# Kernel tuning notes

Measured on AMD Instinct MI355X. Metric: run time of the kernel, lower is better.

Reference implementation:

```python
import jax, jax.numpy as jnp
import numpy as np

N, E, B = 50000, 640000, 4
H, L = 128, 4
NODE_IN, EDGE_IN, COND_IN, NODE_OUT = 12, 4, 10, 3


def _mlp(x, w1, b1, w2, b2):
    # Linear -> ReLU -> Linear
    return jnp.maximum(x @ w1 + b1, 0.0) @ w2 + b2


def setup_inputs() -> dict:
    key = jax.random.key(0)
    keys = iter(jax.random.split(key, 64))

    def p(*shape):
        fan_in = shape[-2] if len(shape) >= 2 else shape[-1]
        return (jax.random.normal(next(keys), shape, jnp.float32) / np.sqrt(fan_in)).astype(jnp.float32)

    inp = {
        "x": jax.random.normal(next(keys), (N, NODE_IN), jnp.float32),
        "edge_index": jax.random.randint(next(keys), (2, E), 0, N),
        "edge_attr": jax.random.normal(next(keys), (E, EDGE_IN), jnp.float32),
        "conditions": jax.random.normal(next(keys), (B, COND_IN), jnp.float32),
        "batch": jnp.sort(jax.random.randint(next(keys), (N,), 0, B)),
        # encoders
        "enc_node_w1": p(NODE_IN, H), "enc_node_b1": jnp.zeros((H,), jnp.float32),
        "enc_node_w2": p(H, H), "enc_node_b2": jnp.zeros((H,), jnp.float32),
        "enc_edge_w1": p(EDGE_IN, H), "enc_edge_b1": jnp.zeros((H,), jnp.float32),
        "enc_edge_w2": p(H, H), "enc_edge_b2": jnp.zeros((H,), jnp.float32),
        "enc_cond_w1": p(COND_IN, H), "enc_cond_b1": jnp.zeros((H,), jnp.float32),
        "enc_cond_w2": p(H, H), "enc_cond_b2": jnp.zeros((H,), jnp.float32),
        # shared MultiheadAttention: with a single key, softmax weight == 1 per head,
        # so output = out_proj(v_proj(kv)); q/k projections cancel exactly (and have
        # identically zero gradient), so only v/out projections are materialized.
        "attn_wv": p(H, H), "attn_bv": jnp.zeros((H,), jnp.float32),
        "attn_wo": p(H, H), "attn_bo": jnp.zeros((H,), jnp.float32),
        # processor layers (stacked over L)
        "pe_w1": p(L, 4 * H, H), "pe_b1": jnp.zeros((L, H), jnp.float32),
        "pe_w2": p(L, H, H), "pe_b2": jnp.zeros((L, H), jnp.float32),
        "pn_w1": p(L, 3 * H, H), "pn_b1": jnp.zeros((L, H), jnp.float32),
        "pn_w2": p(L, H, H), "pn_b2": jnp.zeros((L, H), jnp.float32),
        # decoder
        "dec_w1": p(H, H), "dec_b1": jnp.zeros((H,), jnp.float32),
        "dec_w2": p(H, NODE_OUT), "dec_b2": jnp.zeros((NODE_OUT,), jnp.float32),
    }
    return inp


def reference(x, edge_index, edge_attr, conditions, batch,
              enc_node_w1, enc_node_b1, enc_node_w2, enc_node_b2,
              enc_edge_w1, enc_edge_b1, enc_edge_w2, enc_edge_b2,
              enc_cond_w1, enc_cond_b1, enc_cond_w2, enc_cond_b2,
              attn_wv, attn_bv, attn_wo, attn_bo,
              pe_w1, pe_b1, pe_w2, pe_b2,
              pn_w1, pn_b1, pn_w2, pn_b2,
              dec_w1, dec_b1, dec_w2, dec_b2):
    n = x.shape[0]
    h = _mlp(x, enc_node_w1, enc_node_b1, enc_node_w2, enc_node_b2)           # [N,H]
    e = _mlp(edge_attr, enc_edge_w1, enc_edge_b1, enc_edge_w2, enc_edge_b2)   # [E,H]
    u = _mlp(conditions, enc_cond_w1, enc_cond_b1, enc_cond_w2, enc_cond_b2)  # [B,H]

    row, col = edge_index[0], edge_index[1]
    u_nodes = u[batch]                                                        # [N,H]
    # single-key cross-attention -> softmax over 1 key == 1 -> out_proj(v_proj(u))
    x_cond = (u_nodes @ attn_wv + attn_bv) @ attn_wo + attn_bo               # [N,H], same every layer
    u_edges = u_nodes[row]                                                    # u[batch[row]]

    for l in range(pe_w1.shape[0]):
        # edge update: cat([src, dest, edge_attr, u[batch_e]]) -> MLP
        e = _mlp(jnp.concatenate([h[row], h[col], e, u_edges], axis=1),
                 pe_w1[l], pe_b1[l], pe_w2[l], pe_b2[l])
        # scatter-add aggregation (index_add on row)
        agg = jax.ops.segment_sum(e, row, num_segments=n)                     # [N,H]
        # node update with residual
        h = h + _mlp(jnp.concatenate([h, agg, x_cond], axis=1),
                     pn_w1[l], pn_b1[l], pn_w2[l], pn_b2[l])

    return _mlp(h, dec_w1, dec_b1, dec_w2, dec_b2)                            # [N,node_out]
```

## Files before the change

### kernel.cpp

```cpp
#include <hip/hip_runtime.h>
#include <cstddef>

#define NN 50000
#define NNP 50048
#define NE 640000
#define NB 4
#define H  128
#define NL 4
#define TE 64
#define TEE 128

typedef unsigned int u32;
typedef unsigned short u16;
typedef __attribute__((ext_vector_type(8))) short bf16x8;
typedef __attribute__((ext_vector_type(4))) float f32x4;

__device__ __forceinline__ float bf2f(u16 s) {
    union { u32 u; float f; } v; v.u = ((u32)s) << 16; return v.f;
}
__device__ __forceinline__ u16 f2bf(float f) {
    union { float f; u32 u; } v; v.f = f;
    u32 u = v.u;
    u += 0x7FFF + ((u >> 16) & 1);
    return (u16)(u >> 16);
}
__device__ __forceinline__ void unpack8(uint4 raw, float* d) {
    d[0] = bf2f(raw.x & 0xFFFF); d[1] = bf2f(raw.x >> 16);
    d[2] = bf2f(raw.y & 0xFFFF); d[3] = bf2f(raw.y >> 16);
    d[4] = bf2f(raw.z & 0xFFFF); d[5] = bf2f(raw.z >> 16);
    d[6] = bf2f(raw.w & 0xFFFF); d[7] = bf2f(raw.w >> 16);
}
__device__ __forceinline__ uint4 pack8(const float* s) {
    uint4 pk;
    pk.x = (u32)f2bf(s[0]) | ((u32)f2bf(s[1]) << 16);
    pk.y = (u32)f2bf(s[2]) | ((u32)f2bf(s[3]) << 16);
    pk.z = (u32)f2bf(s[4]) | ((u32)f2bf(s[5]) << 16);
    pk.w = (u32)f2bf(s[6]) | ((u32)f2bf(s[7]) << 16);
    return pk;
}
__device__ __forceinline__ bf16x8 ld_f32_bf8(const float* __restrict__ p) {
    const float4 a = *(const float4*)p;
    const float4 b = *(const float4*)(p + 4);
    bf16x8 r;
    r[0] = (short)f2bf(a.x); r[1] = (short)f2bf(a.y);
    r[2] = (short)f2bf(a.z); r[3] = (short)f2bf(a.w);
    r[4] = (short)f2bf(b.x); r[5] = (short)f2bf(b.y);
    r[6] = (short)f2bf(b.z); r[7] = (short)f2bf(b.w);
    return r;
}

__global__ __launch_bounds__(256) void k_zero(float* __restrict__ p, int n4) {
    const int i = blockIdx.x * 256 + threadIdx.x;
    if (i < n4) ((float4*)p)[i] = make_float4(0.f, 0.f, 0.f, 0.f);
}

__global__ __launch_bounds__(256) void k_hist(const int* __restrict__ rowi,
                                              u32* __restrict__ cnt) {
    const int i = blockIdx.x * 256 + threadIdx.x;
    if (i < NE) atomicAdd(&cnt[rowi[i]], 1u);
}

__global__ __launch_bounds__(1024) void k_scan(u32* __restrict__ cnt) {
    __shared__ u32 part[1024];
    const int t = threadIdx.x;
    const int CHUNK = (NN + 1023) / 1024;
    const int lo = t * CHUNK;
    const int hi = (lo + CHUNK < NN) ? lo + CHUNK : NN;
    u32 s = 0;
    for (int i = lo; i < hi; ++i) s += cnt[i];
    part[t] = s;
    __syncthreads();
    for (int ofs = 1; ofs < 1024; ofs <<= 1) {
        const u32 v = (t >= ofs) ? part[t - ofs] : 0u;
        __syncthreads();
        part[t] += v;
        __syncthreads();
    }
    u32 run = (t == 0) ? 0u : part[t - 1];
    for (int i = lo; i < hi; ++i) { const u32 c = cnt[i]; cnt[i] = run; run += c; }
}

__global__ __launch_bounds__(256) void k_scatter(const int* __restrict__ rowi,
                                                 const int* __restrict__ coli,
                                                 u32* __restrict__ off,
                                                 int* __restrict__ permS,
                                                 int* __restrict__ rowS,
                                                 int* __restrict__ colS) {
    const int i = blockIdx.x * 256 + threadIdx.x;
    if (i < NE) {
        const int r = rowi[i];
        const u32 p = atomicAdd(&off[r], 1u);
        permS[p] = i; rowS[p] = r; colS[p] = coli[i];
    }
}

__global__ __launch_bounds__(256) void k_prep(
    const float* __restrict__ pe_w1, const float* __restrict__ pe_w2,
    const float* __restrict__ pn_w1, const float* __restrict__ pn_w2,
    const float* __restrict__ ew2,   const float* __restrict__ nw2,
    const float* __restrict__ dw1,
    u16* __restrict__ W1t, u16* __restrict__ W2t,
    u16* __restrict__ WaT, u16* __restrict__ WbT,
    u16* __restrict__ Wn1aT, u16* __restrict__ Wn1bT, u16* __restrict__ Wn2T,
    u16* __restrict__ W2et, u16* __restrict__ W2nt, u16* __restrict__ W1dt) {
    const int li = blockIdx.x;
    const float* src; u16* dst;
    switch (blockIdx.y) {
        case 0: src = pe_w1 + ((size_t)li * 512 + 256) * H; dst = W1t  + (size_t)li * H * H; break;
        case 1: src = pe_w2 + (size_t)li * H * H;           dst = W2t  + (size_t)li * H * H; break;
        case 2: src = pe_w1 + (size_t)li * 512 * H;         dst = WaT  + (size_t)li * H * H; break;
        case 3: src = pe_w1 + ((size_t)li * 512 + 128) * H; dst = WbT  + (size_t)li * H * H; break;
        case 4: src = pn_w1 + (size_t)li * 384 * H;         dst = Wn1aT + (size_t)li * H * H; break;
        case 5: src = pn_w1 + ((size_t)li * 384 + 128) * H; dst = Wn1bT + (size_t)li * H * H; break;
        case 6: src = pn_w2 + (size_t)li * H * H;           dst = Wn2T + (size_t)li * H * H; break;
        default:
            if (li == 0)      { src = ew2; dst = W2et; }
            else if (li == 1) { src = nw2; dst = W2nt; }
            else if (li == 2) { src = dw1; dst = W1dt; }
            else return;
            break;
    }
    for (int idx = threadIdx.x; idx < H * H; idx += 256) {
        const int n = idx >> 7, k = idx & 127;
        dst[idx] = f2bf(src[(size_t)k * H + n]);
    }
}

__global__ __launch_bounds__(128) void k_small(
    const float* __restrict__ cond,
    const float* __restrict__ ecw1, const float* __restrict__ ecb1,
    const float* __restrict__ ecw2, const float* __restrict__ ecb2,
    const float* __restrict__ wv, const float* __restrict__ bv,
    const float* __restrict__ wo, const float* __restrict__ bo,
    const float* __restrict__ pe_w1, const float* __restrict__ pe_b1,
    const float* __restrict__ pn_w1, const float* __restrict__ pn_b1,
    float* __restrict__ cbat, float* __restrict__ nbat) {
    __shared__ float tmp[NB][H];
    __shared__ float uL[NB][H];
    __shared__ float xcL[NB][H];
    const int t = threadIdx.x;
    for (int b = 0; b < NB; ++b) {
        float a = ecb1[t];
        for (int k = 0; k < 10; ++k) a = fmaf(cond[b * 10 + k], ecw1[k * H + t], a);
        tmp[b][t] = fmaxf(a, 0.f);
    }
    __syncthreads();
    for (int b = 0; b < NB; ++b) {
        float a = ecb2[t];
        for (int k = 0; k < H; ++k) a = fmaf(tmp[b][k], ecw2[k * H + t], a);
        uL[b][t] = a;
    }
    __syncthreads();
    for (int b = 0; b < NB; ++b) {
        float a = bv[t];
        for (int k = 0; k < H; ++k) a = fmaf(uL[b][k], wv[k * H + t], a);
        tmp[b][t] = a;
    }
    __syncthreads();
    for (int b = 0; b < NB; ++b) {
        float a = bo[t];
        for (int k = 0; k < H; ++k) a = fmaf(tmp[b][k], wo[k * H + t], a);
        xcL[b][t] = a;
    }
    __syncthreads();
    for (int l = 0; l < NL; ++l) {
        const float* w1u = pe_w1 + ((size_t)l * 512 + 384) * H;
        for (int b = 0; b < NB; ++b) {
            float a = pe_b1[l * H + t];
            for (int k = 0; k < H; ++k) a = fmaf(uL[b][k], w1u[k * H + t], a);
            cbat[(l * NB + b) * H + t] = a;
        }
        const float* w1x = pn_w1 + ((size_t)l * 384 + 256) * H;
        for (int b = 0; b < NB; ++b) {
            float a = pn_b1[l * H + t];
            for (int k = 0; k < H; ++k) a = fmaf(xcL[b][k], w1x[k * H + t], a);
            nbat[(l * NB + b) * H + t] = a;
        }
    }
}

__global__ __launch_bounds__(256) void k_enc_e_mfma(
    const float* __restrict__ ea,
    const int* __restrict__ permS,
    const float* __restrict__ w1, const float* __restrict__ b1,
    const u16* __restrict__ W2et, const float* __restrict__ b2,
    u16* __restrict__ e) {
    __shared__ float SI[TE][H + 4];
    const int t = threadIdx.x;
    const long long e0 = (long long)blockIdx.x * TE;
    const int w = t >> 6, l = t & 63;
    const int m16 = l & 15, g = l >> 4;
    const int row = w * 16 + m16;

    const int src = permS[e0 + row];
    const float4 av = *(const float4*)&ea[(size_t)src * 4];

    bf16x8 afrag[4];
#pragma unroll
    for (int ks = 0; ks < 4; ++ks) {
        const int c0 = ks * 32 + g * 8;
        float hv[8];
        {
            const float4 ba = *(const float4*)&b1[c0];
            const float4 bb = *(const float4*)&b1[c0 + 4];
            hv[0] = ba.x; hv[1] = ba.y; hv[2] = ba.z; hv[3] = ba.w;
            hv[4] = bb.x; hv[5] = bb.y; hv[6] = bb.z; hv[7] = bb.w;
        }
#pragma unroll
        for (int k = 0; k < 4; ++k) {
            const float s = (k == 0) ? av.x : (k == 1) ? av.y : (k == 2) ? av.z : av.w;
            const float4 wa = *(const float4*)&w1[k * H + c0];
            const float4 wb = *(const float4*)&w1[k * H + c0 + 4];
            hv[0] = fmaf(s, wa.x, hv[0]); hv[1] = fmaf(s, wa.y, hv[1]);
            hv[2] = fmaf(s, wa.z, hv[2]); hv[3] = fmaf(s, wa.w, hv[3]);
            hv[4] = fmaf(s, wb.x, hv[4]); hv[5] = fmaf(s, wb.y, hv[5]);
            hv[6] = fmaf(s, wb.z, hv[6]); hv[7] = fmaf(s, wb.w, hv[7]);
        }
#pragma unroll
        for (int j = 0; j < 8; ++j) afrag[ks][j] = (short)f2bf(fmaxf(hv[j], 0.f));
    }

    f32x4 acc[8];
#pragma unroll
    for (int nt = 0; nt < 8; ++nt) {
        const float bb = b2[nt * 16 + m16];
        acc[nt][0] = bb; acc[nt][1] = bb; acc[nt][2] = bb; acc[nt][3] = bb;
    }
#pragma unroll
    for (int ks = 0; ks < 4; ++ks) {
#pragma unroll
        for (int nt = 0; nt < 8; ++nt) {
            const bf16x8 bfr =
                *(const bf16x8*)&W2et[(size_t)(nt * 16 + m16) * H + ks * 32 + g * 8];
            acc[nt] = __builtin_amdgcn_mfma_f32_16x16x32_bf16(afrag[ks], bfr, acc[nt], 0, 0, 0);
        }
    }

#pragma unroll
    for (int nt = 0; nt < 8; ++nt)
#pragma unroll
        for (int j = 0; j < 4; ++j)
            SI[w * 16 + g * 4 + j][nt * 16 + m16] = acc[nt][j];
#pragma unroll
    for (int it = 0; it < 4; ++it) {
        const int u = l + it * 64;
        const int j = u >> 4, c8 = (u & 15) * 8;
        *(uint4*)&e[(size_t)(e0 + w * 16 + j) * H + c8] = pack8(&SI[w * 16 + j][c8]);
    }
}

__global__ __launch_bounds__(256) void k_enc_n_mfma(
    const float* __restrict__ x,
    const float* __restrict__ w1, const float* __restrict__ b1,
    const u16* __restrict__ W2nt, const float* __restrict__ b2,
    float* __restrict__ h) {
    __shared__ float SI[TE][H + 4];
    const int t = threadIdx.x;
    const long long n0 = (long long)blockIdx.x * TE;
    const int w = t >> 6, l = t & 63;
    const int m16 = l & 15, g = l >> 4;
    const int row = w * 16 + m16;
    const long long nr = (n0 + row < NN) ? (n0 + row) : (NN - 1);

    float av[12];
    {
        const float4 a0 = *(const float4*)&x[nr * 12];
        const float4 a1 = *(const float4*)&x[nr * 12 + 4];
        const float4 a2 = *(const float4*)&x[nr * 12 + 8];
        av[0] = a0.x; av[1] = a0.y; av[2] = a0.z; av[3] = a0.w;
        av[4] = a1.x; av[5] = a1.y; av[6] = a1.z; av[7] = a1.w;
        av[8] = a2.x; av[9] = a2.y; av[10] = a2.z; av[11] = a2.w;
    }

    bf16x8 afrag[4];
#pragma unroll
    for (int ks = 0; ks < 4; ++ks) {
        const int c0 = ks * 32 + g * 8;
        float hv[8];
        {
            const float4 ba = *(const float4*)&b1[c0];
            const float4 bb = *(const float4*)&b1[c0 + 4];
            hv[0] = ba.x; hv[1] = ba.y; hv[2] = ba.z; hv[3] = ba.w;
            hv[4] = bb.x; hv[5] = bb.y; hv[6] = bb.z; hv[7] = bb.w;
        }
#pragma unroll
        for (int k = 0; k < 12; ++k) {
            const float s = av[k];
            const float4 wa = *(const float4*)&w1[k * H + c0];
            const float4 wb = *(const float4*)&w1[k * H + c0 + 4];
            hv[0] = fmaf(s, wa.x, hv[0]); hv[1] = fmaf(s, wa.y, hv[1]);
            hv[2] = fmaf(s, wa.z, hv[2]); hv[3] = fmaf(s, wa.w, hv[3]);
            hv[4] = fmaf(s, wb.x, hv[4]); hv[5] = fmaf(s, wb.y, hv[5]);
            hv[6] = fmaf(s, wb.z, hv[6]); hv[7] = fmaf(s, wb.w, hv[7]);
        }
#pragma unroll
        for (int j = 0; j < 8; ++j) afrag[ks][j] = (short)f2bf(fmaxf(hv[j], 0.f));
    }

    f32x4 acc[8];
#pragma unroll
    for (int nt = 0; nt < 8; ++nt) {
        const float bb = b2[nt * 16 + m16];
        acc[nt][0] = bb; acc[nt][1] = bb; acc[nt][2] = bb; acc[nt][3] = bb;
    }
#pragma unroll
    for (int ks = 0; ks < 4; ++ks) {
#pragma unroll
        for (int nt = 0; nt < 8; ++nt) {
            const bf16x8 bfr =
                *(const bf16x8*)&W2nt[(size_t)(nt * 16 + m16) * H + ks * 32 + g * 8];
            acc[nt] = __builtin_amdgcn_mfma_f32_16x16x32_bf16(afrag[ks], bfr, acc[nt], 0, 0, 0);
        }
    }

#pragma unroll
    for (int nt = 0; nt < 8; ++nt)
#pragma unroll
        for (int j = 0; j < 4; ++j)
            SI[w * 16 + g * 4 + j][nt * 16 + m16] = acc[nt][j];
    __syncthreads();
    for (int u = t; u < TE * H / 4; u += 256) {
        const int j = u >> 5, c4 = (u & 31) * 4;
        *(float4*)&h[(size_t)(n0 + j) * H + c4] = *(const float4*)&SI[j][c4];
    }
}

__global__ __launch_bounds__(256) void k_gemm_dual_mfma(
    const float* __restrict__ h,
    const u16* __restrict__ WaT, const u16* __restrict__ WbT,
    const float* __restrict__ cbatl, const int* __restrict__ batch,
    u16* __restrict__ Ca, u16* __restrict__ Cb, float* __restrict__ agg) {
    __shared__ u16 SI[TE][H + 8];
    __shared__ float CB[NB][H];
    __shared__ int bL[TE];
    const int t = threadIdx.x;
    const long long n0 = (long long)blockIdx.x * TE;
    const int w = t >> 6, l = t & 63;
    const int m16 = l & 15, g = l >> 4;
    const int row = w * 16 + m16;

    {
        const float4 z4 = make_float4(0.f, 0.f, 0.f, 0.f);
        for (int u = t; u < TE * H / 4; u += 256) {
            const int j = u >> 5, c4 = (u & 31) * 4;
            *(float4*)&agg[(size_t)(n0 + j) * H + c4] = z4;
        }
    }

    if (t < TE) {
        const long long n = n0 + t;
        bL[t] = batch[n < NN ? n : (NN - 1)];
    }
    for (int i = t; i < NB * H; i += 256) ((float*)CB)[i] = cbatl[i];

    bf16x8 afrag[4];
    {
        const float* hp = h + (size_t)(n0 + row) * H + g * 8;
#pragma unroll
        for (int ks = 0; ks < 4; ++ks) afrag[ks] = ld_f32_bf8(hp + ks * 32);
    }
    __syncthreads();

    f32x4 accA[8], accB[8];
#pragma unroll
    for (int nt = 0; nt < 8; ++nt) {
#pragma unroll
        for (int j = 0; j < 4; ++j)
            accA[nt][j] = CB[bL[w * 16 + g * 4 + j]][nt * 16 + m16];
        accB[nt][0] = 0.f; accB[nt][1] = 0.f; accB[nt][2] = 0.f; accB[nt][3] = 0.f;
    }
#pragma unroll
    for (int ks = 0; ks < 4; ++ks) {
#pragma unroll
        for (int nt = 0; nt < 8; ++nt) {
            const size_t off = (size_t)(nt * 16 + m16) * H + ks * 32 + g * 8;
            const bf16x8 ba = *(const bf16x8*)&WaT[off];
            const bf16x8 bb = *(const bf16x8*)&WbT[off];
            accA[nt] = __builtin_amdgcn_mfma_f32_16x16x32_bf16(afrag[ks], ba, accA[nt], 0, 0, 0);
            accB[nt] = __builtin_amdgcn_mfma_f32_16x16x32_bf16(afrag[ks], bb, accB[nt], 0, 0, 0);
        }
    }

#pragma unroll
    for (int s = 0; s < 2; ++s) {
        __syncthreads();
#pragma unroll
        for (int nt = 0; nt < 8; ++nt)
#pragma unroll
            for (int j = 0; j < 4; ++j)
                SI[w * 16 + g * 4 + j][nt * 16 + m16] =
                    f2bf(s ? accB[nt][j] : accA[nt][j]);
        __syncthreads();
        u16* C = s ? Cb : Ca;
        for (int u = t; u < TE * 16; u += 256) {
            const int j = u >> 4, c8 = (u & 15) * 8;
            *(uint4*)&C[(size_t)(n0 + j) * H + c8] = *(const uint4*)&SI[j][c8];
        }
    }
}

template <bool WRITE_E>
__global__ __launch_bounds__(256, 2) void k_edge_mfma(
    const u16* __restrict__ hA, const u16* __restrict__ hB,
    const u16* __restrict__ W1t, const u16* __restrict__ W2t,
    const float* __restrict__ b2,
    const int* __restrict__ rowS, const int* __restrict__ colS,
    u16* __restrict__ e, float* __restrict__ agg) {
    __shared__ u16 SI[TEE][H + 8];
    const int t = threadIdx.x;
    const long long e0 = (long long)blockIdx.x * TEE;
    const int w = t >> 6, l = t & 63;
    const int m16 = l & 15, g = l >> 4;

    bf16x8 af0[4], af1[4];
    {
        const u16* ep0 = e + (size_t)(e0 + w * 32 + m16) * H + g * 8;
        const u16* ep1 = ep0 + 16 * H;
#pragma unroll
        for (int ks = 0; ks < 4; ++ks) {
            af0[ks] = *(const bf16x8*)(ep0 + ks * 32);
            af1[ks] = *(const bf16x8*)(ep1 + ks * 32);
        }
    }

    {
        int rj[8], cj[8];
#pragma unroll
        for (int it = 0; it < 8; ++it) {
            const int j = (l + it * 64) >> 4;
            rj[it] = rowS[e0 + w * 32 + j];
            cj[it] = colS[e0 + w * 32 + j];
        }
        uint4 ga[8], gb[8];
#pragma unroll
        for (int it = 0; it < 8; ++it) {
            const int c8 = ((l + it * 64) & 15) * 8;
            ga[it] = *(const uint4*)&hA[(size_t)rj[it] * H + c8];
            gb[it] = *(const uint4*)&hB[(size_t)cj[it] * H + c8];
        }
#pragma unroll
        for (int it = 0; it < 8; ++it) {
            const int u = l + it * 64;
            const int j = u >> 4, c8 = (u & 15) * 8;
            float va[8], vb[8], sm[8];
            unpack8(ga[it], va);
            unpack8(gb[it], vb);
#pragma unroll
            for (int q = 0; q < 8; ++q) sm[q] = va[q] + vb[q];
            *(uint4*)&SI[w * 32 + j][c8] = pack8(sm);
        }
    }

    f32x4 acc0[8], acc1[8];
#pragma unroll
    for (int nt = 0; nt < 8; ++nt) {
#pragma unroll
        for (int j = 0; j < 4; ++j) {
            acc0[nt][j] = bf2f(SI[w * 32 + g * 4 + j][nt * 16 + m16]);
            acc1[nt][j] = bf2f(SI[w * 32 + 16 + g * 4 + j][nt * 16 + m16]);
        }
    }
#pragma unroll
    for (int ks = 0; ks < 4; ++ks) {
#pragma unroll
        for (int nt = 0; nt < 8; ++nt) {
            const bf16x8 bfr =
                *(const bf16x8*)&W1t[(size_t)(nt * 16 + m16) * H + ks * 32 + g * 8];
            acc0[nt] = __builtin_amdgcn_mfma_f32_16x16x32_bf16(af0[ks], bfr, acc0[nt], 0, 0, 0);
            acc1[nt] = __builtin_amdgcn_mfma_f32_16x16x32_bf16(af1[ks], bfr, acc1[nt], 0, 0, 0);
        }
    }

#pragma unroll
    for (int nt = 0; nt < 8; ++nt)
#pragma unroll
        for (int j = 0; j < 4; ++j) {
            SI[w * 32 + g * 4 + j][nt * 16 + m16]      = f2bf(fmaxf(acc0[nt][j], 0.f));
            SI[w * 32 + 16 + g * 4 + j][nt * 16 + m16] = f2bf(fmaxf(acc1[nt][j], 0.f));
        }

#pragma unroll
    for (int nt = 0; nt < 8; ++nt) {
        const float bb = b2[nt * 16 + m16];
        acc0[nt][0] = bb; acc0[nt][1] = bb; acc0[nt][2] = bb; acc0[nt][3] = bb;
        acc1[nt][0] = bb; acc1[nt][1] = bb; acc1[nt][2] = bb; acc1[nt][3] = bb;
    }
#pragma unroll
    for (int ks = 0; ks < 4; ++ks) {
        const bf16x8 a20 = *(const bf16x8*)&SI[w * 32 + m16][ks * 32 + g * 8];
        const bf16x8 a21 = *(const bf16x8*)&SI[w * 32 + 16 + m16][ks * 32 + g * 8];
#pragma unroll
        for (int nt = 0; nt < 8; ++nt) {
            const bf16x8 bfr =
                *(const bf16x8*)&W2t[(size_t)(nt * 16 + m16) * H + ks * 32 + g * 8];
            acc0[nt] = __builtin_amdgcn_mfma_f32_16x16x32_bf16(a20, bfr, acc0[nt], 0, 0, 0);
            acc1[nt] = __builtin_amdgcn_mfma_f32_16x16x32_bf16(a21, bfr, acc1[nt], 0, 0, 0);
        }
    }

    {
        int r[8];
#pragma unroll
        for (int j = 0; j < 4; ++j) {
            r[j]     = rowS[e0 + w * 32 + g * 4 + j];
            r[4 + j] = rowS[e0 + w * 32 + 16 + g * 4 + j];
        }
#pragma unroll
        for (int nt = 0; nt < 8; ++nt) {
            const int c = nt * 16 + m16;
            float v[8];
#pragma unroll
            for (int j = 0; j < 4; ++j) { v[j] = acc0[nt][j]; v[4 + j] = acc1[nt][j]; }
            float s = v[0];
            int prev = r[0];
#pragma unroll
            for (int j = 1; j < 8; ++j) {
                if (r[j] == prev) s += v[j];
                else { atomicAdd(&agg[(size_t)prev * H + c], s); s = v[j]; prev = r[j]; }
            }
            atomicAdd(&agg[(size_t)prev * H + c], s);
        }
    }

    if (WRITE_E) {
#pragma unroll
        for (int nt = 0; nt < 8; ++nt)
#pragma unroll
            for (int j = 0; j < 4; ++j) {
                SI[w * 32 + g * 4 + j][nt * 16 + m16]      = f2bf(acc0[nt][j]);
                SI[w * 32 + 16 + g * 4 + j][nt * 16 + m16] = f2bf(acc1[nt][j]);
            }
#pragma unroll
        for (int it = 0; it < 8; ++it) {
            const int u = l + it * 64;
            const int j = u >> 4, c8 = (u & 15) * 8;
            *(uint4*)&e[(size_t)(e0 + w * 32 + j) * H + c8] = *(const uint4*)&SI[w * 32 + j][c8];
        }
    }
}

__global__ __launch_bounds__(256) void k_node_mfma(
    const u16* __restrict__ Wn1aT, const u16* __restrict__ Wn1bT,
    const u16* __restrict__ Wn2T, const float* __restrict__ bn2,
    const float* __restrict__ nbatl, const int* __restrict__ batch,
    const float* __restrict__ agg, float* __restrict__ h) {
    __shared__ float SI[TE][H + 4];
    const int t = threadIdx.x;
    const long long n0 = (long long)blockIdx.x * TE;
    const int w = t >> 6, l = t & 63;
    const int m16 = l & 15, g = l >> 4;
    const int row = w * 16 + m16;

    bf16x8 afrag[4];
    {
        const float* hp = h + (size_t)(n0 + row) * H + g * 8;
#pragma unroll
        for (int ks = 0; ks < 4; ++ks) afrag[ks] = ld_f32_bf8(hp + ks * 32);
    }

    int bj[4];
#pragma unroll
    for (int j = 0; j < 4; ++j) {
        const long long n = n0 + w * 16 + g * 4 + j;
        bj[j] = batch[n < NN ? n : (NN - 1)];
    }

    f32x4 acc[8];
#pragma unroll
    for (int nt = 0; nt < 8; ++nt)
#pragma unroll
        for (int j = 0; j < 4; ++j)
            acc[nt][j] = nbatl[(size_t)bj[j] * H + nt * 16 + m16];

#pragma unroll
    for (int ks = 0; ks < 4; ++ks)
#pragma unroll
        for (int nt = 0; nt < 8; ++nt) {
            const bf16x8 bfr =
                *(const bf16x8*)&Wn1aT[(size_t)(nt * 16 + m16) * H + ks * 32 + g * 8];
            acc[nt] = __builtin_amdgcn_mfma_f32_16x16x32_bf16(afrag[ks], bfr, acc[nt], 0, 0, 0);
        }

    {
        const float* ap = agg + (size_t)(n0 + row) * H + g * 8;
#pragma unroll
        for (int ks = 0; ks < 4; ++ks) afrag[ks] = ld_f32_bf8(ap + ks * 32);
    }
#pragma unroll
    for (int ks = 0; ks < 4; ++ks)
#pragma unroll
        for (int nt = 0; nt < 8; ++nt) {
            const bf16x8 bfr =
                *(const bf16x8*)&Wn1bT[(size_t)(nt * 16 + m16) * H + ks * 32 + g * 8];
            acc[nt] = __builtin_amdgcn_mfma_f32_16x16x32_bf16(afrag[ks], bfr, acc[nt], 0, 0, 0);
        }

#pragma unroll
    for (int nt = 0; nt < 8; ++nt)
#pragma unroll
        for (int j = 0; j < 4; ++j)
            SI[w * 16 + g * 4 + j][nt * 16 + m16] = fmaxf(acc[nt][j], 0.f);

#pragma unroll
    for (int nt = 0; nt < 8; ++nt) {
        const float bb = bn2[nt * 16 + m16];
        acc[nt][0] = bb; acc[nt][1] = bb; acc[nt][2] = bb; acc[nt][3] = bb;
    }
#pragma unroll
    for (int ks = 0; ks < 4; ++ks) {
        bf16x8 a2;
        const float* hp = &SI[w * 16 + m16][ks * 32 + g * 8];
#pragma unroll
        for (int j = 0; j < 8; ++j) a2[j] = (short)f2bf(hp[j]);
#pragma unroll
        for (int nt = 0; nt < 8; ++nt) {
            const bf16x8 bfr =
                *(const bf16x8*)&Wn2T[(size_t)(nt * 16 + m16) * H + ks * 32 + g * 8];
            acc[nt] = __builtin_amdgcn_mfma_f32_16x16x32_bf16(a2, bfr, acc[nt], 0, 0, 0);
        }
    }

#pragma unroll
    for (int nt = 0; nt < 8; ++nt)
#pragma unroll
        for (int j = 0; j < 4; ++j)
            SI[w * 16 + g * 4 + j][nt * 16 + m16] = acc[nt][j];

#pragma unroll
    for (int it = 0; it < 8; ++it) {
        const int u = l + it * 64;
        const int j = u >> 5, c4 = (u & 31) * 4;
        float4 hv = *(const float4*)&h[(size_t)(n0 + w * 16 + j) * H + c4];
        const float4 sv = *(const float4*)&SI[w * 16 + j][c4];
        hv.x += sv.x; hv.y += sv.y; hv.z += sv.z; hv.w += sv.w;
        *(float4*)&h[(size_t)(n0 + w * 16 + j) * H + c4] = hv;
    }
}

__global__ __launch_bounds__(256) void k_dec_mfma(
    const float* __restrict__ h,
    const u16* __restrict__ W1dt, const float* __restrict__ b1,
    const float* __restrict__ w2, const float* __restrict__ b2,
    float* __restrict__ out) {
    __shared__ float SI[TE][H + 4];
    const int t = threadIdx.x;
    const long long n0 = (long long)blockIdx.x * TE;
    const int w = t >> 6, l = t & 63;
    const int m16 = l & 15, g = l >> 4;
    const int row = w * 16 + m16;

    bf16x8 afrag[4];
    {
        const float* hp = h + (size_t)(n0 + row) * H + g * 8;
#pragma unroll
        for (int ks = 0; ks < 4; ++ks) afrag[ks] = ld_f32_bf8(hp + ks * 32);
    }

    f32x4 acc[8];
#pragma unroll
    for (int nt = 0; nt < 8; ++nt) {
        const float bb = b1[nt * 16 + m16];
        acc[nt][0] = bb; acc[nt][1] = bb; acc[nt][2] = bb; acc[nt][3] = bb;
    }
#pragma unroll
    for (int ks = 0; ks < 4; ++ks) {
#pragma unroll
        for (int nt = 0; nt < 8; ++nt) {
            const bf16x8 bfr =
                *(const bf16x8*)&W1dt[(size_t)(nt * 16 + m16) * H + ks * 32 + g * 8];
            acc[nt] = __builtin_amdgcn_mfma_f32_16x16x32_bf16(afrag[ks], bfr, acc[nt], 0, 0, 0);
        }
    }

#pragma unroll
    for (int nt = 0; nt < 8; ++nt)
#pragma unroll
        for (int j = 0; j < 4; ++j)
            SI[w * 16 + g * 4 + j][nt * 16 + m16] = fmaxf(acc[nt][j], 0.f);
    __syncthreads();

    if (t < TE * 3) {
        const int n = t / 3, c = t - n * 3;
        if (n0 + n < NN) {
            float v = b2[c];
            for (int k = 0; k < H; ++k) v = fmaf(SI[n][k], w2[k * 3 + c], v);
            out[(size_t)(n0 + n) * 3 + c] = v;
        }
    }
}

extern "C" void kernel_launch(void* const* d_in, const int* in_sizes, int n_in,
                              void* d_out, int out_size, void* d_ws, size_t ws_size,
                              hipStream_t stream) {
    const float* x          = (const float*)d_in[0];
    const int*   edge_index = (const int*)d_in[1];
    const float* edge_attr  = (const float*)d_in[2];
    const float* cond       = (const float*)d_in[3];
    const int*   batch      = (const int*)d_in[4];
    const float* enc_node_w1 = (const float*)d_in[5];
    const float* enc_node_b1 = (const float*)d_in[6];
    const float* enc_node_w2 = (const float*)d_in[7];
    const float* enc_node_b2 = (const float*)d_in[8];
    const float* enc_edge_w1 = (const float*)d_in[9];
    const float* enc_edge_b1 = (const float*)d_in[10];
    const float* enc_edge_w2 = (const float*)d_in[11];
    const float* enc_edge_b2 = (const float*)d_in[12];
    const float* enc_cond_w1 = (const float*)d_in[13];
    const float* enc_cond_b1 = (const float*)d_in[14];
    const float* enc_cond_w2 = (const float*)d_in[15];
    const float* enc_cond_b2 = (const float*)d_in[16];
    const float* attn_wv = (const float*)d_in[17];
    const float* attn_bv = (const float*)d_in[18];
    const float* attn_wo = (const float*)d_in[19];
    const float* attn_bo = (const float*)d_in[20];
    const float* pe_w1 = (const float*)d_in[21];
    const float* pe_b1 = (const float*)d_in[22];
    const float* pe_w2 = (const float*)d_in[23];
    const float* pe_b2 = (const float*)d_in[24];
    const float* pn_w1 = (const float*)d_in[25];
    const float* pn_b1 = (const float*)d_in[26];
    const float* pn_w2 = (const float*)d_in[27];
    const float* pn_b2 = (const float*)d_in[28];
    const float* dec_w1 = (const float*)d_in[29];
    const float* dec_b1 = (const float*)d_in[30];
    const float* dec_w2 = (const float*)d_in[31];
    const float* dec_b2 = (const float*)d_in[32];

    u16*   e    = (u16*)d_ws;
    float* h    = (float*)((char*)d_ws + (size_t)NE * H * 2);
    float* agg  = h + (size_t)NNP * H;
    u16*   hA   = (u16*)(agg + (size_t)NNP * H);
    u16*   hB   = hA + (size_t)NNP * H;
    float* cbat = (float*)(hB + (size_t)NNP * H);
    float* nbat = cbat + NL * NB * H;
    u16*   W1t   = (u16*)(nbat + NL * NB * H);
    u16*   W2t   = W1t  + (size_t)NL * H * H;
    u16*   WaT   = W2t  + (size_t)NL * H * H;
    u16*   WbT   = WaT  + (size_t)NL * H * H;
    u16*   Wn1aT = WbT  + (size_t)NL * H * H;
    u16*   Wn1bT = Wn1aT + (size_t)NL * H * H;
    u16*   Wn2T  = Wn1bT + (size_t)NL * H * H;
    u16*   W2et  = Wn2T + (size_t)NL * H * H;
    u16*   W2nt  = W2et + (size_t)H * H;
    u16*   W1dt  = W2nt + (size_t)H * H;
    u32*   cnt   = (u32*)(W1dt + (size_t)H * H);
    int*   permS = (int*)(cnt + NNP);
    int*   rowS  = permS + NE;
    int*   colS  = rowS + NE;

    const int* rowi = edge_index;
    const int* coli = edge_index + NE;
    float* out = (float*)d_out;

    k_zero<<<(NNP / 4 + 255) / 256, 256, 0, stream>>>((float*)cnt, NNP / 4);
    k_hist<<<NE / 256, 256, 0, stream>>>(rowi, cnt);
    k_scan<<<1, 1024, 0, stream>>>(cnt);
    k_scatter<<<NE / 256, 256, 0, stream>>>(rowi, coli, cnt, permS, rowS, colS);

    k_prep<<<dim3(NL, 8), 256, 0, stream>>>(pe_w1, pe_w2, pn_w1, pn_w2,
                                            enc_edge_w2, enc_node_w2, dec_w1,
                                            W1t, W2t, WaT, WbT,
                                            Wn1aT, Wn1bT, Wn2T, W2et, W2nt, W1dt);
    k_small<<<1, 128, 0, stream>>>(cond, enc_cond_w1, enc_cond_b1, enc_cond_w2, enc_cond_b2,
                                   attn_wv, attn_bv, attn_wo, attn_bo,
                                   pe_w1, pe_b1, pn_w1, pn_b1, cbat, nbat);
    k_enc_n_mfma<<<NNP / TE, 256, 0, stream>>>(
        x, enc_node_w1, enc_node_b1, W2nt, enc_node_b2, h);
    k_enc_e_mfma<<<NE / TE, 256, 0, stream>>>(
        edge_attr, permS, enc_edge_w1, enc_edge_b1, W2et, enc_edge_b2, e);

    for (int l = 0; l < NL; ++l) {
        k_gemm_dual_mfma<<<NNP / TE, 256, 0, stream>>>(
            h, WaT + (size_t)l * H * H, WbT + (size_t)l * H * H,
            cbat + l * NB * H, batch, hA, hB, agg);
        if (l < NL - 1)
            k_edge_mfma<true><<<NE / TEE, 256, 0, stream>>>(
                hA, hB, W1t + (size_t)l * H * H, W2t + (size_t)l * H * H,
                pe_b2 + l * H, rowS, colS, e, agg);
        else
            k_edge_mfma<false><<<NE / TEE, 256, 0, stream>>>(
                hA, hB, W1t + (size_t)l * H * H, W2t + (size_t)l * H * H,
                pe_b2 + l * H, rowS, colS, e, agg);
        k_node_mfma<<<NNP / TE, 256, 0, stream>>>(
            Wn1aT + (size_t)l * H * H, Wn1bT + (size_t)l * H * H,
            Wn2T + (size_t)l * H * H, pn_b2 + l * H,
            nbat + l * NB * H, batch, agg, h);
    }
    k_dec_mfma<<<NNP / TE, 256, 0, stream>>>(h, W1dt, dec_b1, dec_w2, dec_b2, out);
}
```

Before: 2.304 ms.

## Fuse next-layer dual GEMM and decoder into node update kernel

The node-update kernel now keeps the updated h tile in shared memory and immediately computes the next layer's per-node projections (hA/hB) and zeroes agg, replacing the separate dual-GEMM launch. For the last layer it runs the decoder MLP in the same kernel. This removes re-reading h from global memory and several kernel launches per forward, at the cost of higher register pressure from the extra accumulators in one kernel.

Result: no change. 2.304 ms (-0.0%).

```diff
diff --git a/kernel.cpp b/kernel.cpp
--- a/kernel.cpp
+++ b/kernel.cpp
@@ -539,14 +539,12 @@
     }
 }
 
-__global__ __launch_bounds__(256) void k_node_mfma(
+__device__ __forceinline__ void node_update_body(
+    float (*SI)[H + 4], const long long n0, const int t,
     const u16* __restrict__ Wn1aT, const u16* __restrict__ Wn1bT,
     const u16* __restrict__ Wn2T, const float* __restrict__ bn2,
     const float* __restrict__ nbatl, const int* __restrict__ batch,
-    const float* __restrict__ agg, float* __restrict__ h) {
-    __shared__ float SI[TE][H + 4];
-    const int t = threadIdx.x;
-    const long long n0 = (long long)blockIdx.x * TE;
+    const float* __restrict__ agg, float* __restrict__ h, int bj[4]) {
     const int w = t >> 6, l = t & 63;
     const int m16 = l & 15, g = l >> 4;
     const int row = w * 16 + m16;
@@ -558,7 +556,6 @@
         for (int ks = 0; ks < 4; ++ks) afrag[ks] = ld_f32_bf8(hp + ks * 32);
     }
 
-    int bj[4];
 #pragma unroll
     for (int j = 0; j < 4; ++j) {
         const long long n = n0 + w * 16 + g * 4 + j;
@@ -634,33 +631,116 @@
         const float4 sv = *(const float4*)&SI[w * 16 + j][c4];
         hv.x += sv.x; hv.y += sv.y; hv.z += sv.z; hv.w += sv.w;
         *(float4*)&h[(size_t)(n0 + w * 16 + j) * H + c4] = hv;
-    }
-}
-
-__global__ __launch_bounds__(256) void k_dec_mfma(
-    const float* __restrict__ h,
-    const u16* __restrict__ W1dt, const float* __restrict__ b1,
-    const float* __restrict__ w2, const float* __restrict__ b2,
+        *(float4*)&SI[w * 16 + j][c4] = hv;
+    }
+}
+
+__global__ __launch_bounds__(256) void k_node_next(
+    const u16* __restrict__ Wn1aT, const u16* __restrict__ Wn1bT,
+    const u16* __restrict__ Wn2T, const float* __restrict__ bn2,
+    const float* __restrict__ nbatl, const int* __restrict__ batch,
+    float* __restrict__ agg, float* __restrict__ h,
+    const u16* __restrict__ WaT2, const u16* __restrict__ WbT2,
+    const float* __restrict__ cbat2,
+    u16* __restrict__ Ca, u16* __restrict__ Cb) {
+    __shared__ float SI[TE][H + 4];
+    const int t = threadIdx.x;
+    const long long n0 = (long long)blockIdx.x * TE;
+    const int w = t >> 6, l = t & 63;
+    const int m16 = l & 15, g = l >> 4;
+    int bj[4];
+
+    node_update_body(SI, n0, t, Wn1aT, Wn1bT, Wn2T, bn2, nbatl, batch, agg, h, bj);
+
+    bf16x8 afn[4];
+#pragma unroll
+    for (int ks = 0; ks < 4; ++ks) {
+        const float* hp = &SI[w * 16 + m16][ks * 32 + g * 8];
+#pragma unroll
+        for (int j = 0; j < 8; ++j) afn[ks][j] = (short)f2bf(hp[j]);
+    }
+
+    {
+        const float4 z4 = make_float4(0.f, 0.f, 0.f, 0.f);
+#pragma unroll
+        for (int it = 0; it < 8; ++it) {
+            const int u = l + it * 64;
+            const int j = u >> 5, c4 = (u & 31) * 4;
+            *(float4*)&agg[(size_t)(n0 + w * 16 + j) * H + c4] = z4;
+        }
+    }
+
+    f32x4 aA[8], aB[8];
+#pragma unroll
+    for (int nt = 0; nt < 8; ++nt) {
+#pragma unroll
+        for (int j = 0; j < 4; ++j)
+            aA[nt][j] = cbat2[(size_t)bj[j] * H + nt * 16 + m16];
+        aB[nt][0] = 0.f; aB[nt][1] = 0.f; aB[nt][2] = 0.f; aB[nt][3] = 0.f;
+    }
+#pragma unroll
+    for (int ks = 0; ks < 4; ++ks) {
+#pragma unroll
+        for (int nt = 0; nt < 8; ++nt) {
+            const size_t off = (size_t)(nt * 16 + m16) * H + ks * 32 + g * 8;
+            const bf16x8 ba = *(const bf16x8*)&WaT2[off];
+            const bf16x8 bb = *(const bf16x8*)&WbT2[off];
+            aA[nt] = __builtin_amdgcn_mfma_f32_16x16x32_bf16(afn[ks], ba, aA[nt], 0, 0, 0);
+            aB[nt] = __builtin_amdgcn_mfma_f32_16x16x32_bf16(afn[ks], bb, aB[nt], 0, 0, 0);
+        }
+    }
+
+    u16* SIu = (u16*)&SI[0][0];
+    const int RSU = 2 * (H + 4);
+#pragma unroll
+    for (int s = 0; s < 2; ++s) {
+#pragma unroll
+        for (int nt = 0; nt < 8; ++nt)
+#pragma unroll
+            for (int j = 0; j < 4; ++j)
+                SIu[(size_t)(w * 16 + g * 4 + j) * RSU + nt * 16 + m16] =
+                    f2bf(s ? aB[nt][j] : aA[nt][j]);
+        u16* C = s ? Cb : Ca;
+#pragma unroll
+        for (int it = 0; it < 4; ++it) {
+            const int u = l + it * 64;
+            const int j = u >> 4, c8 = (u & 15) * 8;
+            *(uint4*)&C[(size_t)(n0 + w * 16 + j) * H + c8] =
+                *(const uint4*)&SIu[(size_t)(w * 16 + j) * RSU + c8];
+        }
+    }
+}
+
+__global__ __launch_bounds__(256) void k_node_last(
+    const u16* __restrict__ Wn1aT, const u16* __restrict__ Wn1bT,
+    const u16* __restrict__ Wn2T, const float* __restrict__ bn2,
+    const float* __restrict__ nbatl, const int* __restrict__ batch,
+    const float* __restrict__ agg, float* __restrict__ h,
+    const u16* __restrict__ W1dt, const float* __restrict__ db1,
+    const float* __restrict__ dw2, const float* __restrict__ db2,
     float* __restrict__ out) {
     __shared__ float SI[TE][H + 4];
     const int t = threadIdx.x;
     const long long n0 = (long long)blockIdx.x * TE;
     const int w = t >> 6, l = t & 63;
     const int m16 = l & 15, g = l >> 4;
-    const int row = w * 16 + m16;
-
-    bf16x8 afrag[4];
-    {
-        const float* hp = h + (size_t)(n0 + row) * H + g * 8;
-#pragma unroll
-        for (int ks = 0; ks < 4; ++ks) afrag[ks] = ld_f32_bf8(hp + ks * 32);
-    }
-
-    f32x4 acc[8];
+    int bj[4];
+
+    node_update_body(SI, n0, t, Wn1aT, Wn1bT, Wn2T, bn2, nbatl, batch, agg, h, bj);
+
+    bf16x8 afn[4];
+#pragma unroll
+    for (int ks = 0; ks < 4; ++ks) {
+        const float* hp = &SI[w * 16 + m16][ks * 32 + g * 8];
+#pragma unroll
+        for (int j = 0; j < 8; ++j) afn[ks][j] = (short)f2bf(hp[j]);
+    }
+
+    f32x4 ad[8];
 #pragma unroll
     for (int nt = 0; nt < 8; ++nt) {
-        const float bb = b1[nt * 16 + m16];
-        acc[nt][0] = bb; acc[nt][1] = bb; acc[nt][2] = bb; acc[nt][3] = bb;
+        const float bb = db1[nt * 16 + m16];
+        ad[nt][0] = bb; ad[nt][1] = bb; ad[nt][2] = bb; ad[nt][3] = bb;
     }
 #pragma unroll
     for (int ks = 0; ks < 4; ++ks) {
@@ -668,7 +748,7 @@
         for (int nt = 0; nt < 8; ++nt) {
             const bf16x8 bfr =
                 *(const bf16x8*)&W1dt[(size_t)(nt * 16 + m16) * H + ks * 32 + g * 8];
-            acc[nt] = __builtin_amdgcn_mfma_f32_16x16x32_bf16(afrag[ks], bfr, acc[nt], 0, 0, 0);
+            ad[nt] = __builtin_amdgcn_mfma_f32_16x16x32_bf16(afn[ks], bfr, ad[nt], 0, 0, 0);
         }
     }
 
@@ -676,14 +756,14 @@
     for (int nt = 0; nt < 8; ++nt)
 #pragma unroll
         for (int j = 0; j < 4; ++j)
-            SI[w * 16 + g * 4 + j][nt * 16 + m16] = fmaxf(acc[nt][j], 0.f);
+            SI[w * 16 + g * 4 + j][nt * 16 + m16] = fmaxf(ad[nt][j], 0.f);
     __syncthreads();
 
     if (t < TE * 3) {
         const int n = t / 3, c = t - n * 3;
         if (n0 + n < NN) {
-            float v = b2[c];
-            for (int k = 0; k < H; ++k) v = fmaf(SI[n][k], w2[k * 3 + c], v);
+            float v = db2[c];
+            for (int k = 0; k < H; ++k) v = fmaf(SI[n][k], dw2[k * 3 + c], v);
             out[(size_t)(n0 + n) * 3 + c] = v;
         }
     }
@@ -769,22 +849,29 @@
     k_enc_e_mfma<<<NE / TE, 256, 0, stream>>>(
         edge_attr, permS, enc_edge_w1, enc_edge_b1, W2et, enc_edge_b2, e);
 
+    k_gemm_dual_mfma<<<NNP / TE, 256, 0, stream>>>(
+        h, WaT, WbT, cbat, batch, hA, hB, agg);
+
     for (int l = 0; l < NL; ++l) {
-        k_gemm_dual_mfma<<<NNP / TE, 256, 0, stream>>>(
-            h, WaT + (size_t)l * H * H, WbT + (size_t)l * H * H,
-            cbat + l * NB * H, batch, hA, hB, agg);
-        if (l < NL - 1)
+        if (l < NL - 1) {
             k_edge_mfma<true><<<NE / TEE, 256, 0, stream>>>(
                 hA, hB, W1t + (size_t)l * H * H, W2t + (size_t)l * H * H,
                 pe_b2 + l * H, rowS, colS, e, agg);
-        else
+            k_node_next<<<NNP / TE, 256, 0, stream>>>(
+                Wn1aT + (size_t)l * H * H, Wn1bT + (size_t)l * H * H,
+                Wn2T + (size_t)l * H * H, pn_b2 + l * H,
+                nbat + l * NB * H, batch, agg, h,
+                WaT + (size_t)(l + 1) * H * H, WbT + (size_t)(l + 1) * H * H,
+                cbat + (l + 1) * NB * H, hA, hB);
+        } else {
             k_edge_mfma<false><<<NE / TEE, 256, 0, stream>>>(
                 hA, hB, W1t + (size_t)l * H * H, W2t + (size_t)l * H * H,
                 pe_b2 + l * H, rowS, colS, e, agg);
-        k_node_mfma<<<NNP / TE, 256, 0, stream>>>(
-            Wn1aT + (size_t)l * H * H, Wn1bT + (size_t)l * H * H,
-            Wn2T + (size_t)l * H * H, pn_b2 + l * H,
-            nbat + l * NB * H, batch, agg, h);
-    }
-    k_dec_mfma<<<NNP / TE, 256, 0, stream>>>(h, W1dt, dec_b1, dec_w2, dec_b2, out);
-}
+            k_node_last<<<NNP / TE, 256, 0, stream>>>(
+                Wn1aT + (size_t)l * H * H, Wn1bT + (size_t)l * H * H,
+                Wn2T + (size_t)l * H * H, pn_b2 + l * H,
+                nbat + l * NB * H, batch, agg, h,
+                W1dt, dec_b1, dec_w2, dec_b2, out);
+        }
+    }
+}
```
